# Performance work log

Measured on AMD Instinct MI355X. Metric: run time of the kernel, lower is better.

The kernel has to match this reference:

```python
import jax, jax.numpy as jnp
import numpy as np

IOU_THRESHOLD = 0.7
TOP_K = 100
TAKE_N = 10
EPS = 1e-8


def _iou(proposals, gts):
    # proposals: [B,H,W,A,4] (x1,y1,x2,y2); gts: [G,4] -> iou [B,H,W,G,A]
    p = proposals[:, :, :, None, :, :]          # [B,H,W,1,A,4]
    g = gts[:, None, :]                          # [G,1,4]
    ix1 = jnp.maximum(p[..., 0], g[..., 0])      # [B,H,W,G,A]
    iy1 = jnp.maximum(p[..., 1], g[..., 1])
    ix2 = jnp.minimum(p[..., 2], g[..., 2])
    iy2 = jnp.minimum(p[..., 3], g[..., 3])
    inter = jnp.clip(ix2 - ix1, 0.0) * jnp.clip(iy2 - iy1, 0.0)
    area_p = (p[..., 2] - p[..., 0]) * (p[..., 3] - p[..., 1])
    area_g = (g[..., 2] - g[..., 0]) * (g[..., 3] - g[..., 1])
    return inter / (area_p + area_g - inter + EPS)


def _sample_masked(key, mask, n):
    # uniformly pick n True positions (static shape; pads arbitrarily if < n True)
    score = jnp.where(mask, jax.random.uniform(key, mask.shape), -1.0)
    _, sel = jax.lax.top_k(score, n)
    return sel


def setup_inputs() -> dict:
    key = jax.random.key(0)
    k1, k2, k3, k5 = jax.random.split(key, 4)
    B, H, W, A, G, K = 8, 100, 100, 9, 50, 18
    raw = jax.random.uniform(k1, (B, H, W, A, 4), dtype=jnp.float32)
    xy = raw[..., :2]
    proposals = jnp.concatenate([xy, xy + raw[..., 2:] * 0.2 + 0.01], axis=-1)
    cls_prob = jax.random.uniform(k2, (B, H, W, K), dtype=jnp.float32)
    anchor_prob = jax.random.uniform(k3, (B, H, W, K), dtype=jnp.float32)
    # gt boxes copied from proposals (guarantees some IoU > threshold matches)
    flat = proposals.reshape(-1, 4)
    stride = flat.shape[0] // G
    gt_proposals = flat[::stride][:G]
    gt_cls = jax.random.randint(k5, (G,), 0, 21, dtype=jnp.int32)
    return {"proposals": proposals, "cls_prob": cls_prob, "anchor_prob": anchor_prob,
            "gt_proposals": gt_proposals, "gt_cls": gt_cls}


def reference(proposals, cls_prob, anchor_prob, gt_proposals, gt_cls):
    kp, kn = jax.random.split(jax.random.key(42))
    iou = _iou(proposals, gt_proposals)               # [B,H,W,G,A]
    B, H, W, G, A = iou.shape
    flat_iou = iou.reshape(-1)
    vals, idxs = jax.lax.top_k(flat_iou, TOP_K)
    pos_mask = vals > IOU_THRESHOLD
    sel = _sample_masked(kp, pos_mask, TAKE_N)
    flat_sel = idxs[sel]
    b, h, w, g, a = jnp.unravel_index(flat_sel, iou.shape)
    proposals_index = jnp.stack([b, h, w, g, a], axis=-1)       # [N,5]
    positive_proposals = proposals[b, h, w, a]                  # [N,4]
    positive_cls_prob = cls_prob[b, h, w]                       # [N,K]
    positive_gt_proposals = gt_proposals[g]                     # [N,4]
    positive_gt_cls = gt_cls[g]                                 # [N]
    positive_anchor = a                                         # [N]
    positive_anchor_cls = anchor_prob[b, h, w]                  # [N,K]
    iou_per_position = iou.max(axis=(3, 4))                     # [B,H,W]
    neg_mask = (iou_per_position < IOU_THRESHOLD).reshape(-1)
    nsel = _sample_masked(kn, neg_mask, TAKE_N)
    nb, nh, nw = jnp.unravel_index(nsel, (B, H, W))
    negative_index = jnp.stack([nb, nh, nw], axis=-1)           # [N,3]
    negative_cls_prob = cls_prob[nb, nh, nw]                    # [N,K]
    return (proposals_index, positive_proposals, positive_cls_prob,
            positive_gt_proposals, positive_gt_cls, positive_anchor,
            positive_anchor_cls, negative_index, negative_cls_prob)
```

## Files before the change

kernel.cpp:

```cpp
#include <hip/hip_runtime.h>

constexpr int B = 8, H = 100, W = 100, A = 9, G = 50, K = 18;
constexpr int NPROP = B * H * W * A;
constexpr int NPOS  = B * H * W;
constexpr int CAND_CAP = 65536;
constexpr float THR = 0.7f;

#define JAX_PARTITIONABLE 1

#define TPB 576
#define NB_P 625
#define TPC 512
#define BLK_CAND 1024
#define REFINE_THR 384

__device__ int g_candCount;
__device__ unsigned int g_hist[4096];
__device__ unsigned long long g_cand[CAND_CAP];
__device__ unsigned long long g_negtop[NB_P * 10];

__device__ __forceinline__ unsigned int rotl32(unsigned int x, int r) {
    return (x << r) | (x >> (32 - r));
}
__device__ __forceinline__ void tfr(unsigned int& x0, unsigned int& x1, int r) {
    x0 += x1; x1 = rotl32(x1, r); x1 ^= x0;
}
__device__ void threefry2x32(unsigned int k0, unsigned int k1,
                             unsigned int c0, unsigned int c1,
                             unsigned int& o0, unsigned int& o1) {
    unsigned int ks2 = k0 ^ k1 ^ 0x1BD11BDAu;
    unsigned int x0 = c0 + k0, x1 = c1 + k1;
    tfr(x0,x1,13); tfr(x0,x1,15); tfr(x0,x1,26); tfr(x0,x1, 6);
    x0 += k1;  x1 += ks2 + 1u;
    tfr(x0,x1,17); tfr(x0,x1,29); tfr(x0,x1,16); tfr(x0,x1,24);
    x0 += ks2; x1 += k0 + 2u;
    tfr(x0,x1,13); tfr(x0,x1,15); tfr(x0,x1,26); tfr(x0,x1, 6);
    x0 += k0;  x1 += k1 + 3u;
    tfr(x0,x1,17); tfr(x0,x1,29); tfr(x0,x1,16); tfr(x0,x1,24);
    x0 += k1;  x1 += ks2 + 4u;
    tfr(x0,x1,13); tfr(x0,x1,15); tfr(x0,x1,26); tfr(x0,x1, 6);
    x0 += ks2; x1 += k0 + 5u;
    o0 = x0; o1 = x1;
}

__device__ void derive_keys(unsigned int& kp0, unsigned int& kp1,
                            unsigned int& kn0, unsigned int& kn1) {
#if JAX_PARTITIONABLE
    threefry2x32(0u, 42u, 0u, 0u, kp0, kp1);
    threefry2x32(0u, 42u, 0u, 1u, kn0, kn1);
#else
    unsigned int a0, b0, a1, b1;
    threefry2x32(0u, 42u, 0u, 2u, a0, b0);
    threefry2x32(0u, 42u, 1u, 3u, a1, b1);
    kp0 = a0; kp1 = a1; kn0 = b0; kn1 = b1;
#endif
}

__device__ float jax_uniform(unsigned int k0, unsigned int k1, unsigned int i, unsigned int n) {
    unsigned int bits;
#if JAX_PARTITIONABLE
    unsigned int o0, o1;
    threefry2x32(k0, k1, 0u, i, o0, o1);
    bits = o0 ^ o1;
#else
    unsigned int half = n >> 1;
    unsigned int o0, o1;
    if (i < half) { threefry2x32(k0, k1, i, i + half, o0, o1); bits = o0; }
    else          { threefry2x32(k0, k1, i - half, i, o0, o1); bits = o1; }
#endif
    unsigned int fb = (bits >> 9) | 0x3F800000u;
    return __uint_as_float(fb) - 1.0f;
}

__global__ __launch_bounds__(TPB) void prod_kernel(
        const float* __restrict__ proposals, const float* __restrict__ gtp) {
    __shared__ float  s41[G];
    __shared__ unsigned int sflag[128];
    __shared__ unsigned long long scand[BLK_CAND];
    __shared__ unsigned long long snk[128];
    __shared__ unsigned long long wk[10];
    __shared__ int sh_cnt, sh_base;

    const int t = threadIdx.x;
    const int bid = blockIdx.x;
    const float4* gtp4 = reinterpret_cast<const float4*>(gtp);

    if (t < G) {
        float4 gb = gtp4[t];
        s41[t] = __fmul_rn(0.41f, __fmul_rn(__fsub_rn(gb.z, gb.x), __fsub_rn(gb.w, gb.y)));
    }
    if (t < 128) sflag[t] = 0u;
    if (t == 0) sh_cnt = 0;
    __syncthreads();

    int p0 = bid * 1152 + t;
    float4 x0 = reinterpret_cast<const float4*>(proposals)[p0];
    float4 x1 = reinterpret_cast<const float4*>(proposals)[p0 + 576];
    float ap0 = __fmul_rn(__fsub_rn(x0.z, x0.x), __fsub_rn(x0.w, x0.y));
    float ap1 = __fmul_rn(__fsub_rn(x1.z, x1.x), __fsub_rn(x1.w, x1.y));
    float a41_0 = __fmul_rn(0.41f, ap0);
    float a41_1 = __fmul_rn(0.41f, ap1);
    int li = t / 9, a = t - li * 9;
    int base0 = (bid * 128 + li) * (G * A) + a;
    int base1 = (bid * 128 + 64 + li) * (G * A) + a;
    unsigned f0 = 0u, f1 = 0u;

    for (int g = 0; g < G; ++g) {
        float4 gb = gtp4[g];
        float sg41 = s41[g];
        {
            float dx = __fsub_rn(fminf(x0.z, gb.z), fmaxf(x0.x, gb.x));
            float dy = __fsub_rn(fminf(x0.w, gb.w), fmaxf(x0.y, gb.y));
            float inter = __fmul_rn(fmaxf(dx, 0.0f), fmaxf(dy, 0.0f));
            if (inter > __fadd_rn(a41_0, sg41)) {
                float ag = __fmul_rn(__fsub_rn(gb.z, gb.x), __fsub_rn(gb.w, gb.y));
                float den = __fadd_rn(__fsub_rn(__fadd_rn(ap0, ag), inter), 1e-8f);
                float iou = __fdiv_rn(inter, den);
                if (iou >= THR) f0 = 1u;
                if (iou > THR) {
                    unsigned int delta = __float_as_uint(iou) - 0x3F333334u;
                    unsigned int idx = (unsigned int)(base0 + g * A);
                    unsigned long long key = ((unsigned long long)delta << 32)
                                           | (unsigned long long)(~idx);
                    int s = atomicAdd(&sh_cnt, 1);
                    if (s < BLK_CAND) scand[s] = key;
                    else { int gs = atomicAdd(&g_candCount, 1);
                           if (gs < CAND_CAP) { g_cand[gs] = key;
                               atomicAdd(&g_hist[(unsigned)(key >> 43)], 1u); } }
                }
            }
        }
        {
            float dx = __fsub_rn(fminf(x1.z, gb.z), fmaxf(x1.x, gb.x));
            float dy = __fsub_rn(fminf(x1.w, gb.w), fmaxf(x1.y, gb.y));
            float inter = __fmul_rn(fmaxf(dx, 0.0f), fmaxf(dy, 0.0f));
            if (inter > __fadd_rn(a41_1, sg41)) {
                float ag = __fmul_rn(__fsub_rn(gb.z, gb.x), __fsub_rn(gb.w, gb.y));
                float den = __fadd_rn(__fsub_rn(__fadd_rn(ap1, ag), inter), 1e-8f);
                float iou = __fdiv_rn(inter, den);
                if (iou >= THR) f1 = 1u;
                if (iou > THR) {
                    unsigned int delta = __float_as_uint(iou) - 0x3F333334u;
                    unsigned int idx = (unsigned int)(base1 + g * A);
                    unsigned long long key = ((unsigned long long)delta << 32)
                                           | (unsigned long long)(~idx);
                    int s = atomicAdd(&sh_cnt, 1);
                    if (s < BLK_CAND) scand[s] = key;
                    else { int gs = atomicAdd(&g_candCount, 1);
                           if (gs < CAND_CAP) { g_cand[gs] = key;
                               atomicAdd(&g_hist[(unsigned)(key >> 43)], 1u); } }
                }
            }
        }
    }
    if (f0) atomicOr(&sflag[li], 1u);
    if (f1) atomicOr(&sflag[li + 64], 1u);
    if (t < 10) wk[t] = 0ull;
    __syncthreads();

    int cnt = sh_cnt; if (cnt > BLK_CAND) cnt = BLK_CAND;
    if (t == 0) sh_base = atomicAdd(&g_candCount, cnt);
    if (t < 128) {
        unsigned int kp0, kp1, kn0, kn1;
        derive_keys(kp0, kp1, kn0, kn1);
        unsigned long long key = 0ull;
        if (sflag[t] == 0u) {
            unsigned int pos = (unsigned)(bid * 128 + t);
            float u = jax_uniform(kn0, kn1, pos, (unsigned)NPOS);
            key = ((unsigned long long)__float_as_uint(u) << 32)
                | (unsigned long long)(~pos);
        }
        snk[t] = key;
    }
    __syncthreads();
    int base = sh_base;
    for (int i = t; i < cnt; i += TPB) {
        int gi = base + i;
        if (gi < CAND_CAP) {
            unsigned long long k2 = scand[i];
            g_cand[gi] = k2;
            atomicAdd(&g_hist[(unsigned)(k2 >> 43)], 1u);
        }
    }
    if (t < 128) {
        unsigned long long k2 = snk[t];
        if (k2 != 0ull) {
            int r = 0;
            for (int j = 0; j < 128; ++j) r += (snk[j] > k2) ? 1 : 0;
            if (r < 10) wk[r] = k2;
        }
    }
    __syncthreads();
    if (t < 10) g_negtop[bid * 10 + t] = wk[t];
}

__global__ __launch_bounds__(TPC) void cons_kernel(
        const float* __restrict__ proposals, const float* __restrict__ cls_prob,
        const float* __restrict__ anchor_prob, const float* __restrict__ gtp,
        const int* __restrict__ gtc, float* __restrict__ out) {
    __shared__ unsigned int hist[4096];
    __shared__ int sfx[256];
    __shared__ unsigned long long cbuf[BLK_CAND];
    __shared__ unsigned long long lst[100];
    __shared__ unsigned long long skeys[128];
    __shared__ unsigned long long swin[10];
    __shared__ unsigned long long wred[8];
    __shared__ int selIdx[10];
    __shared__ int s_g[10], s_a[10], s_pos[10], s_bb[10], s_hh[10], s_ww[10], s_npos[10];
    __shared__ int sh_d, sh_before, sh_d2, sh_cnt;

    const int t = threadIdx.x;

    if (blockIdx.x == 0) {
        int C = g_candCount;
        if (C > CAND_CAP) C = CAND_CAP;
        int needTotal = C < 100 ? C : 100;
        int M = 0;

        if (C <= 256) {
            for (int i = t; i < C; i += TPC) cbuf[i] = g_cand[i];
            __syncthreads();
            M = C;
        } else {
            int need = needTotal;
            for (int i = t; i < 4096; i += TPC) hist[i] = g_hist[i];
            __syncthreads();
            if (t < 256) {
                int ps = 0;
                for (int q = 0; q < 16; ++q) ps += (int)hist[t * 16 + q];
                sfx[t] = ps;
            }
            __syncthreads();
            if (t < 64) {
                int lane = t;
                int c0 = sfx[4*lane+0], c1 = sfx[4*lane+1], c2 = sfx[4*lane+2], c3 = sfx[4*lane+3];
                int tot = c0 + c1 + c2 + c3;
                int acc = tot;
                for (int s = 1; s < 64; s <<= 1) {
                    int u = __shfl_down(acc, s);
                    if (lane + s < 64) acc += u;
                }
                int aboveG = acc - tot;
                int CS3 = aboveG;
                int CS2 = CS3 + c3;
                int CS1 = CS2 + c2;
                int CS0 = CS1 + c1;
                int CSv[4] = {CS0, CS1, CS2, CS3};
                int cv[4]  = {c0, c1, c2, c3};
#pragma unroll
                for (int j = 0; j < 4; ++j) {
                    if (CSv[j] < need && CSv[j] + cv[j] >= need) {
                        int cum = CSv[j];
                        for (int b = (4*lane+j)*16 + 15; b >= (4*lane+j)*16; --b) {
                            int h = (int)hist[b];
                            if (cum + h >= need) { sh_d = b; sh_before = cum; break; }
                            cum += h;
                        }
                    }
                }
            }
            __syncthreads();
            int d = sh_d, sb = sh_before;
            int tie = (int)hist[d];
            unsigned long long lo = ((unsigned long long)(unsigned)d) << 43;
            int total = sb + tie;

            if (total > REFINE_THR) {
                __syncthreads();
                for (int i = t; i < 2048; i += TPC) hist[i] = 0u;
                __syncthreads();
                for (int i = t; i < C; i += TPC) {
                    unsigned long long k2 = g_cand[i];
                    if ((unsigned)(k2 >> 43) == (unsigned)d)
                        atomicAdd(&hist[(unsigned)(k2 >> 32) & 0x7FFu], 1u);
                }
                __syncthreads();
                if (t == 0) {
                    int cum = sb;
                    for (int b = 2047; b >= 0; --b) {
                        int h = (int)hist[b];
                        if (cum + h >= need) { sh_d2 = b; break; }
                        cum += h;
                    }
                }
                __syncthreads();
                lo |= ((unsigned long long)(unsigned)sh_d2) << 32;
            }

            if (t == 0) sh_cnt = 0;
            __syncthreads();
            for (int i = t; i < C; i += TPC) {
                unsigned long long k2 = g_cand[i];
                if (k2 >= lo) {
                    int s2 = atomicAdd(&sh_cnt, 1);
                    if (s2 < BLK_CAND) cbuf[s2] = k2;
                }
            }
            __syncthreads();
            M = sh_cnt < BLK_CAND ? sh_cnt : BLK_CAND;
        }

        for (int i = t; i < M; i += TPC) {
            unsigned long long ki = cbuf[i];
            int r = 0;
            for (int j = 0; j < M; ++j) r += (cbuf[j] > ki) ? 1 : 0;
            if (r < needTotal) lst[r] = ki;
        }
        __syncthreads();

        unsigned int kp0, kp1, kn0, kn1;
        derive_keys(kp0, kp1, kn0, kn1);
        if (t < needTotal) {
            float u = jax_uniform(kp0, kp1, (unsigned)t, 100u);
            skeys[t] = ((unsigned long long)__float_as_uint(u) << 32)
                     | (unsigned long long)(~(unsigned)t);
        }
        __syncthreads();
        if (t < needTotal) {
            unsigned long long s = skeys[t];
            int r = 0;
            for (int j = 0; j < needTotal; ++j) r += (skeys[j] > s) ? 1 : 0;
            if (r < 10) selIdx[r] = t;
        }
        __syncthreads();

        if (t < 10) {
            unsigned long long key = lst[selIdx[t]];
            unsigned int fidx = ~(unsigned int)(key & 0xFFFFFFFFull);
            int aa = fidx % A; unsigned int rest = fidx / A;
            int gg = rest % G; rest /= G;
            int ww = rest % W; rest /= W;
            int hh = rest % H; int bb = rest / H;
            s_a[t] = aa; s_g[t] = gg; s_ww[t] = ww; s_hh[t] = hh; s_bb[t] = bb;
            s_pos[t] = (bb * H + hh) * W + ww;
        }
        __syncthreads();

        if (t < 510) {
            int e = t;
            float v;
            if (e < 50)       { int i = e / 5, f = e - 5 * i;
                                v = (float)((f==0)?s_bb[i]:(f==1)?s_hh[i]:(f==2)?s_ww[i]:(f==3)?s_g[i]:s_a[i]); }
            else if (e < 90)  { int u = e - 50, i = u >> 2, q = u & 3;
                                v = proposals[(size_t)(s_pos[i] * A + s_a[i]) * 4 + q]; }
            else if (e < 270) { int u = e - 90, i = u / 18, q = u - 18 * i;
                                v = cls_prob[(size_t)s_pos[i] * K + q]; }
            else if (e < 310) { int u = e - 270, i = u >> 2, q = u & 3;
                                v = gtp[s_g[i] * 4 + q]; }
            else if (e < 320) { v = (float)gtc[s_g[e - 310]]; }
            else if (e < 330) { v = (float)s_a[e - 320]; }
            else              { int u = e - 330, i = u / 18, q = u - 18 * i;
                                v = anchor_prob[(size_t)s_pos[i] * K + q]; }
            out[e] = v;
        }

        __syncthreads();
        for (int i = t; i < 4096; i += TPC) g_hist[i] = 0u;
        if (t == 0) g_candCount = 0;

    } else {
        unsigned long long top[10];
#pragma unroll
        for (int j = 0; j < 10; ++j) top[j] = 0ull;
        for (int i = t; i < NB_P * 10; i += TPC) {
            unsigned long long key = g_negtop[i];
#pragma unroll
            for (int j = 0; j < 10; ++j) {
                if (key > top[j]) { unsigned long long tmp = top[j]; top[j] = key; key = tmp; }
            }
        }
        int lane = t & 63, wid = t >> 6;
        for (int r = 0; r < 10; ++r) {
            unsigned long long w = top[0];
            for (int s = 1; s < 64; s <<= 1) {
                unsigned long long o = __shfl_xor(w, s);
                if (o > w) w = o;
            }
            if (lane == 0) wred[wid] = w;
            __syncthreads();
            unsigned long long m = wred[0];
#pragma unroll
            for (int i = 1; i < 8; ++i) { unsigned long long x = wred[i]; if (x > m) m = x; }
            if (t == 0) swin[r] = m;
            if (top[0] == m) {
#pragma unroll
                for (int j = 0; j < 9; ++j) top[j] = top[j + 1];
                top[9] = 0ull;
            }
            __syncthreads();
        }
        if (t < 10) s_npos[t] = (int)(~(unsigned int)(swin[t] & 0xFFFFFFFFull));
        __syncthreads();

        if (t < 210) {
            int e = 510 + t;
            float v;
            if (e < 540) { int u = e - 510, i = u / 3, f = u - 3 * i; int p = s_npos[i];
                           v = (float)((f==0) ? (p / (H * W)) : (f==1) ? ((p / W) % H) : (p % W)); }
            else         { int u = e - 540, i = u / 18, q = u - 18 * i;
                           v = cls_prob[(size_t)s_npos[i] * K + q]; }
            out[e] = v;
        }
    }
}

extern "C" void kernel_launch(void* const* d_in, const int* in_sizes, int n_in,
                              void* d_out, int out_size, void* d_ws, size_t ws_size,
                              hipStream_t stream) {
    const float* proposals   = (const float*)d_in[0];
    const float* cls_prob    = (const float*)d_in[1];
    const float* anchor_prob = (const float*)d_in[2];
    const float* gtp         = (const float*)d_in[3];
    const int*   gtc         = (const int*)d_in[4];
    float* out = (float*)d_out;

    prod_kernel<<<NB_P, TPB, 0, stream>>>(proposals, gtp);
    cons_kernel<<<2, TPC, 0, stream>>>(proposals, cls_prob, anchor_prob, gtp, gtc, out);
}
```

Before: 44.09 us.

## Fuse producer and consumer into one kernel with binned candidate buckets

Merges the IoU producer kernel and the two-block consumer kernel into a single launch. The extra last block spin-waits on a global completion counter before running the top-k selection. Candidates are now written straight into per-histogram-bin global buckets, replacing the per-block shared staging plus compaction. The consumer therefore scans only the bins at or above the threshold bin instead of the whole candidate list. This removes a kernel launch boundary and the full rescan, at the cost of many global atomics per candidate. It also relies on the waiting block not starving the producers, and the positive and negative selection paths are now serialized in one block.

```diff
diff --git a/kernel.cpp b/kernel.cpp
--- a/kernel.cpp
+++ b/kernel.cpp
@@ -3,20 +3,23 @@
 constexpr int B = 8, H = 100, W = 100, A = 9, G = 50, K = 18;
 constexpr int NPROP = B * H * W * A;
 constexpr int NPOS  = B * H * W;
-constexpr int CAND_CAP = 65536;
 constexpr float THR = 0.7f;
 
 #define JAX_PARTITIONABLE 1
 
 #define TPB 576
 #define NB_P 625
-#define TPC 512
+#define GRID (NB_P + 1)
+#define NBIN 2560
+#define BINCAP 512
+#define SPILL_CAP 16384
 #define BLK_CAND 1024
-#define REFINE_THR 384
-
-__device__ int g_candCount;
-__device__ unsigned int g_hist[4096];
-__device__ unsigned long long g_cand[CAND_CAP];
+
+__device__ unsigned int g_bincnt[NBIN];
+__device__ int g_spillCount;
+__device__ int g_done;
+__device__ unsigned long long g_bins[(size_t)NBIN * BINCAP];
+__device__ unsigned long long g_spill[SPILL_CAP];
 __device__ unsigned long long g_negtop[NB_P * 10];
 
 __device__ __forceinline__ unsigned int rotl32(unsigned int x, int r) {
@@ -72,335 +75,327 @@
     return __uint_as_float(fb) - 1.0f;
 }
 
-__global__ __launch_bounds__(TPB) void prod_kernel(
-        const float* __restrict__ proposals, const float* __restrict__ gtp) {
-    __shared__ float  s41[G];
-    __shared__ unsigned int sflag[128];
-    __shared__ unsigned long long scand[BLK_CAND];
-    __shared__ unsigned long long snk[128];
-    __shared__ unsigned long long wk[10];
-    __shared__ int sh_cnt, sh_base;
-
-    const int t = threadIdx.x;
-    const int bid = blockIdx.x;
-    const float4* gtp4 = reinterpret_cast<const float4*>(gtp);
-
-    if (t < G) {
-        float4 gb = gtp4[t];
-        s41[t] = __fmul_rn(0.41f, __fmul_rn(__fsub_rn(gb.z, gb.x), __fsub_rn(gb.w, gb.y)));
-    }
-    if (t < 128) sflag[t] = 0u;
-    if (t == 0) sh_cnt = 0;
-    __syncthreads();
-
-    int p0 = bid * 1152 + t;
-    float4 x0 = reinterpret_cast<const float4*>(proposals)[p0];
-    float4 x1 = reinterpret_cast<const float4*>(proposals)[p0 + 576];
-    float ap0 = __fmul_rn(__fsub_rn(x0.z, x0.x), __fsub_rn(x0.w, x0.y));
-    float ap1 = __fmul_rn(__fsub_rn(x1.z, x1.x), __fsub_rn(x1.w, x1.y));
-    float a41_0 = __fmul_rn(0.41f, ap0);
-    float a41_1 = __fmul_rn(0.41f, ap1);
-    int li = t / 9, a = t - li * 9;
-    int base0 = (bid * 128 + li) * (G * A) + a;
-    int base1 = (bid * 128 + 64 + li) * (G * A) + a;
-    unsigned f0 = 0u, f1 = 0u;
-
-    for (int g = 0; g < G; ++g) {
-        float4 gb = gtp4[g];
-        float sg41 = s41[g];
-        {
-            float dx = __fsub_rn(fminf(x0.z, gb.z), fmaxf(x0.x, gb.x));
-            float dy = __fsub_rn(fminf(x0.w, gb.w), fmaxf(x0.y, gb.y));
-            float inter = __fmul_rn(fmaxf(dx, 0.0f), fmaxf(dy, 0.0f));
-            if (inter > __fadd_rn(a41_0, sg41)) {
-                float ag = __fmul_rn(__fsub_rn(gb.z, gb.x), __fsub_rn(gb.w, gb.y));
-                float den = __fadd_rn(__fsub_rn(__fadd_rn(ap0, ag), inter), 1e-8f);
-                float iou = __fdiv_rn(inter, den);
-                if (iou >= THR) f0 = 1u;
-                if (iou > THR) {
-                    unsigned int delta = __float_as_uint(iou) - 0x3F333334u;
-                    unsigned int idx = (unsigned int)(base0 + g * A);
-                    unsigned long long key = ((unsigned long long)delta << 32)
-                                           | (unsigned long long)(~idx);
-                    int s = atomicAdd(&sh_cnt, 1);
-                    if (s < BLK_CAND) scand[s] = key;
-                    else { int gs = atomicAdd(&g_candCount, 1);
-                           if (gs < CAND_CAP) { g_cand[gs] = key;
-                               atomicAdd(&g_hist[(unsigned)(key >> 43)], 1u); } }
-                }
-            }
-        }
-        {
-            float dx = __fsub_rn(fminf(x1.z, gb.z), fmaxf(x1.x, gb.x));
-            float dy = __fsub_rn(fminf(x1.w, gb.w), fmaxf(x1.y, gb.y));
-            float inter = __fmul_rn(fmaxf(dx, 0.0f), fmaxf(dy, 0.0f));
-            if (inter > __fadd_rn(a41_1, sg41)) {
-                float ag = __fmul_rn(__fsub_rn(gb.z, gb.x), __fsub_rn(gb.w, gb.y));
-                float den = __fadd_rn(__fsub_rn(__fadd_rn(ap1, ag), inter), 1e-8f);
-                float iou = __fdiv_rn(inter, den);
-                if (iou >= THR) f1 = 1u;
-                if (iou > THR) {
-                    unsigned int delta = __float_as_uint(iou) - 0x3F333334u;
-                    unsigned int idx = (unsigned int)(base1 + g * A);
-                    unsigned long long key = ((unsigned long long)delta << 32)
-                                           | (unsigned long long)(~idx);
-                    int s = atomicAdd(&sh_cnt, 1);
-                    if (s < BLK_CAND) scand[s] = key;
-                    else { int gs = atomicAdd(&g_candCount, 1);
-                           if (gs < CAND_CAP) { g_cand[gs] = key;
-                               atomicAdd(&g_hist[(unsigned)(key >> 43)], 1u); } }
-                }
-            }
-        }
-    }
-    if (f0) atomicOr(&sflag[li], 1u);
-    if (f1) atomicOr(&sflag[li + 64], 1u);
-    if (t < 10) wk[t] = 0ull;
-    __syncthreads();
-
-    int cnt = sh_cnt; if (cnt > BLK_CAND) cnt = BLK_CAND;
-    if (t == 0) sh_base = atomicAdd(&g_candCount, cnt);
-    if (t < 128) {
-        unsigned int kp0, kp1, kn0, kn1;
-        derive_keys(kp0, kp1, kn0, kn1);
-        unsigned long long key = 0ull;
-        if (sflag[t] == 0u) {
-            unsigned int pos = (unsigned)(bid * 128 + t);
-            float u = jax_uniform(kn0, kn1, pos, (unsigned)NPOS);
-            key = ((unsigned long long)__float_as_uint(u) << 32)
-                | (unsigned long long)(~pos);
-        }
-        snk[t] = key;
-    }
-    __syncthreads();
-    int base = sh_base;
-    for (int i = t; i < cnt; i += TPB) {
-        int gi = base + i;
-        if (gi < CAND_CAP) {
-            unsigned long long k2 = scand[i];
-            g_cand[gi] = k2;
-            atomicAdd(&g_hist[(unsigned)(k2 >> 43)], 1u);
-        }
-    }
-    if (t < 128) {
-        unsigned long long k2 = snk[t];
-        if (k2 != 0ull) {
-            int r = 0;
-            for (int j = 0; j < 128; ++j) r += (snk[j] > k2) ? 1 : 0;
-            if (r < 10) wk[r] = k2;
-        }
-    }
-    __syncthreads();
-    if (t < 10) g_negtop[bid * 10 + t] = wk[t];
-}
-
-__global__ __launch_bounds__(TPC) void cons_kernel(
+__device__ __forceinline__ void emit_candidate(float iou, unsigned int idx) {
+    unsigned int delta = __float_as_uint(iou) - 0x3F333334u;
+    unsigned long long key = ((unsigned long long)delta << 32)
+                           | (unsigned long long)(~idx);
+    unsigned int bin = (unsigned int)(key >> 43);
+    unsigned int slot = atomicAdd(&g_bincnt[bin], 1u);
+    if (slot < BINCAP) g_bins[(size_t)bin * BINCAP + slot] = key;
+    else { int gs = atomicAdd(&g_spillCount, 1);
+           if (gs < SPILL_CAP) g_spill[gs] = key; }
+}
+
+__global__ __launch_bounds__(TPB) void fused_kernel(
         const float* __restrict__ proposals, const float* __restrict__ cls_prob,
         const float* __restrict__ anchor_prob, const float* __restrict__ gtp,
         const int* __restrict__ gtc, float* __restrict__ out) {
-    __shared__ unsigned int hist[4096];
+    __shared__ float  s41[G];
+    __shared__ unsigned int sflag[128];
+    __shared__ unsigned long long snk[128];
+    __shared__ unsigned long long wk[10];
+    __shared__ unsigned int hist[NBIN];
     __shared__ int sfx[256];
+    __shared__ unsigned int rhist[2048];
     __shared__ unsigned long long cbuf[BLK_CAND];
     __shared__ unsigned long long lst[100];
     __shared__ unsigned long long skeys[128];
     __shared__ unsigned long long swin[10];
-    __shared__ unsigned long long wred[8];
+    __shared__ unsigned long long wred[9];
     __shared__ int selIdx[10];
     __shared__ int s_g[10], s_a[10], s_pos[10], s_bb[10], s_hh[10], s_ww[10], s_npos[10];
-    __shared__ int sh_d, sh_before, sh_d2, sh_cnt;
+    __shared__ int sh_d, sh_before, sh_C, sh_d2, sh_cnt, sh_ovf;
 
     const int t = threadIdx.x;
-
-    if (blockIdx.x == 0) {
-        int C = g_candCount;
-        if (C > CAND_CAP) C = CAND_CAP;
-        int needTotal = C < 100 ? C : 100;
-        int M = 0;
-
-        if (C <= 256) {
-            for (int i = t; i < C; i += TPC) cbuf[i] = g_cand[i];
-            __syncthreads();
-            M = C;
-        } else {
-            int need = needTotal;
-            for (int i = t; i < 4096; i += TPC) hist[i] = g_hist[i];
-            __syncthreads();
-            if (t < 256) {
-                int ps = 0;
-                for (int q = 0; q < 16; ++q) ps += (int)hist[t * 16 + q];
-                sfx[t] = ps;
-            }
-            __syncthreads();
-            if (t < 64) {
-                int lane = t;
-                int c0 = sfx[4*lane+0], c1 = sfx[4*lane+1], c2 = sfx[4*lane+2], c3 = sfx[4*lane+3];
-                int tot = c0 + c1 + c2 + c3;
-                int acc = tot;
-                for (int s = 1; s < 64; s <<= 1) {
-                    int u = __shfl_down(acc, s);
-                    if (lane + s < 64) acc += u;
+    const int bid = blockIdx.x;
+    const float4* gtp4 = reinterpret_cast<const float4*>(gtp);
+
+    if (bid < NB_P) {
+        if (t < G) {
+            float4 gb = gtp4[t];
+            s41[t] = __fmul_rn(0.41f, __fmul_rn(__fsub_rn(gb.z, gb.x), __fsub_rn(gb.w, gb.y)));
+        }
+        if (t < 128) sflag[t] = 0u;
+        __syncthreads();
+
+        int p0 = bid * 1152 + t;
+        float4 x0 = reinterpret_cast<const float4*>(proposals)[p0];
+        float4 x1 = reinterpret_cast<const float4*>(proposals)[p0 + 576];
+        float ap0 = __fmul_rn(__fsub_rn(x0.z, x0.x), __fsub_rn(x0.w, x0.y));
+        float ap1 = __fmul_rn(__fsub_rn(x1.z, x1.x), __fsub_rn(x1.w, x1.y));
+        float a41_0 = __fmul_rn(0.41f, ap0);
+        float a41_1 = __fmul_rn(0.41f, ap1);
+        int li = t / 9, a = t - li * 9;
+        int base0 = (bid * 128 + li) * (G * A) + a;
+        int base1 = (bid * 128 + 64 + li) * (G * A) + a;
+        unsigned f0 = 0u, f1 = 0u;
+
+        for (int g = 0; g < G; ++g) {
+            float4 gb = gtp4[g];
+            float sg41 = s41[g];
+            {
+                float dx = __fsub_rn(fminf(x0.z, gb.z), fmaxf(x0.x, gb.x));
+                float dy = __fsub_rn(fminf(x0.w, gb.w), fmaxf(x0.y, gb.y));
+                float inter = __fmul_rn(fmaxf(dx, 0.0f), fmaxf(dy, 0.0f));
+                if (inter > __fadd_rn(a41_0, sg41)) {
+                    float ag = __fmul_rn(__fsub_rn(gb.z, gb.x), __fsub_rn(gb.w, gb.y));
+                    float den = __fadd_rn(__fsub_rn(__fadd_rn(ap0, ag), inter), 1e-8f);
+                    float iou = __fdiv_rn(inter, den);
+                    if (iou >= THR) f0 = 1u;
+                    if (iou > THR) emit_candidate(iou, (unsigned int)(base0 + g * A));
                 }
-                int aboveG = acc - tot;
-                int CS3 = aboveG;
-                int CS2 = CS3 + c3;
-                int CS1 = CS2 + c2;
-                int CS0 = CS1 + c1;
-                int CSv[4] = {CS0, CS1, CS2, CS3};
-                int cv[4]  = {c0, c1, c2, c3};
+            }
+            {
+                float dx = __fsub_rn(fminf(x1.z, gb.z), fmaxf(x1.x, gb.x));
+                float dy = __fsub_rn(fminf(x1.w, gb.w), fmaxf(x1.y, gb.y));
+                float inter = __fmul_rn(fmaxf(dx, 0.0f), fmaxf(dy, 0.0f));
+                if (inter > __fadd_rn(a41_1, sg41)) {
+                    float ag = __fmul_rn(__fsub_rn(gb.z, gb.x), __fsub_rn(gb.w, gb.y));
+                    float den = __fadd_rn(__fsub_rn(__fadd_rn(ap1, ag), inter), 1e-8f);
+                    float iou = __fdiv_rn(inter, den);
+                    if (iou >= THR) f1 = 1u;
+                    if (iou > THR) emit_candidate(iou, (unsigned int)(base1 + g * A));
+                }
+            }
+        }
+        if (f0) atomicOr(&sflag[li], 1u);
+        if (f1) atomicOr(&sflag[li + 64], 1u);
+        if (t < 10) wk[t] = 0ull;
+        __syncthreads();
+
+        if (t < 128) {
+            unsigned int kp0, kp1, kn0, kn1;
+            derive_keys(kp0, kp1, kn0, kn1);
+            unsigned long long key = 0ull;
+            if (sflag[t] == 0u) {
+                unsigned int pos = (unsigned)(bid * 128 + t);
+                float u = jax_uniform(kn0, kn1, pos, (unsigned)NPOS);
+                key = ((unsigned long long)__float_as_uint(u) << 32)
+                    | (unsigned long long)(~pos);
+            }
+            snk[t] = key;
+        }
+        __syncthreads();
+        if (t < 128) {
+            unsigned long long k2 = snk[t];
+            if (k2 != 0ull) {
+                int r = 0;
+                for (int j = 0; j < 128; ++j) r += (snk[j] > k2) ? 1 : 0;
+                if (r < 10) wk[r] = k2;
+            }
+        }
+        __syncthreads();
+        if (t < 10) g_negtop[bid * 10 + t] = wk[t];
+        __syncthreads();
+        if (t == 0)
+            __hip_atomic_fetch_add(&g_done, 1, __ATOMIC_RELEASE, __HIP_MEMORY_SCOPE_AGENT);
+        return;
+    }
+
+    if (t == 0) {
+        while (__hip_atomic_load(&g_done, __ATOMIC_ACQUIRE, __HIP_MEMORY_SCOPE_AGENT) < NB_P)
+            __builtin_amdgcn_s_sleep(8);
+    }
+    __syncthreads();
+
+    for (int i = t; i < NBIN; i += TPB) hist[i] = g_bincnt[i];
+    if (t == 0) { sh_d = NBIN - 1; sh_before = 0; sh_ovf = 0; sh_cnt = 0; }
+    __syncthreads();
+    if (t < 256) {
+        int ps = 0;
+        for (int q = 0; q < 10; ++q) ps += (int)hist[t * 10 + q];
+        sfx[t] = ps;
+    }
+    __syncthreads();
+    if (t < 64) {
+        int lane = t;
+        int c0 = sfx[4*lane+0], c1 = sfx[4*lane+1], c2 = sfx[4*lane+2], c3 = sfx[4*lane+3];
+        int tot = c0 + c1 + c2 + c3;
+        int acc = tot;
+        for (int s = 1; s < 64; s <<= 1) {
+            int u = __shfl_down(acc, s);
+            if (lane + s < 64) acc += u;
+        }
+        int C = __shfl(acc, 0);
+        if (lane == 0) sh_C = C;
+        int need = C < 100 ? C : 100;
+        int aboveG = acc - tot;
+        int CS3 = aboveG;
+        int CS2 = CS3 + c3;
+        int CS1 = CS2 + c2;
+        int CS0 = CS1 + c1;
+        int CSv[4] = {CS0, CS1, CS2, CS3};
+        int cv[4]  = {c0, c1, c2, c3};
 #pragma unroll
-                for (int j = 0; j < 4; ++j) {
-                    if (CSv[j] < need && CSv[j] + cv[j] >= need) {
-                        int cum = CSv[j];
-                        for (int b = (4*lane+j)*16 + 15; b >= (4*lane+j)*16; --b) {
-                            int h = (int)hist[b];
-                            if (cum + h >= need) { sh_d = b; sh_before = cum; break; }
-                            cum += h;
-                        }
-                    }
+        for (int j = 0; j < 4; ++j) {
+            if (CSv[j] < need && CSv[j] + cv[j] >= need) {
+                int cum = CSv[j];
+                int cbin = 4*lane + j;
+                for (int b = cbin*10 + 9; b >= cbin*10; --b) {
+                    int h = (int)hist[b];
+                    if (cum + h >= need) { sh_d = b; sh_before = cum; break; }
+                    cum += h;
                 }
             }
-            __syncthreads();
-            int d = sh_d, sb = sh_before;
-            int tie = (int)hist[d];
-            unsigned long long lo = ((unsigned long long)(unsigned)d) << 43;
-            int total = sb + tie;
-
-            if (total > REFINE_THR) {
-                __syncthreads();
-                for (int i = t; i < 2048; i += TPC) hist[i] = 0u;
-                __syncthreads();
-                for (int i = t; i < C; i += TPC) {
-                    unsigned long long k2 = g_cand[i];
-                    if ((unsigned)(k2 >> 43) == (unsigned)d)
-                        atomicAdd(&hist[(unsigned)(k2 >> 32) & 0x7FFu], 1u);
-                }
-                __syncthreads();
-                if (t == 0) {
-                    int cum = sb;
-                    for (int b = 2047; b >= 0; --b) {
-                        int h = (int)hist[b];
-                        if (cum + h >= need) { sh_d2 = b; break; }
-                        cum += h;
-                    }
-                }
-                __syncthreads();
-                lo |= ((unsigned long long)(unsigned)sh_d2) << 32;
-            }
-
-            if (t == 0) sh_cnt = 0;
-            __syncthreads();
-            for (int i = t; i < C; i += TPC) {
-                unsigned long long k2 = g_cand[i];
-                if (k2 >= lo) {
-                    int s2 = atomicAdd(&sh_cnt, 1);
-                    if (s2 < BLK_CAND) cbuf[s2] = k2;
-                }
-            }
-            __syncthreads();
-            M = sh_cnt < BLK_CAND ? sh_cnt : BLK_CAND;
-        }
-
-        for (int i = t; i < M; i += TPC) {
-            unsigned long long ki = cbuf[i];
-            int r = 0;
-            for (int j = 0; j < M; ++j) r += (cbuf[j] > ki) ? 1 : 0;
-            if (r < needTotal) lst[r] = ki;
-        }
-        __syncthreads();
-
-        unsigned int kp0, kp1, kn0, kn1;
-        derive_keys(kp0, kp1, kn0, kn1);
-        if (t < needTotal) {
-            float u = jax_uniform(kp0, kp1, (unsigned)t, 100u);
-            skeys[t] = ((unsigned long long)__float_as_uint(u) << 32)
-                     | (unsigned long long)(~(unsigned)t);
-        }
-        __syncthreads();
-        if (t < needTotal) {
-            unsigned long long s = skeys[t];
-            int r = 0;
-            for (int j = 0; j < needTotal; ++j) r += (skeys[j] > s) ? 1 : 0;
-            if (r < 10) selIdx[r] = t;
-        }
-        __syncthreads();
-
-        if (t < 10) {
-            unsigned long long key = lst[selIdx[t]];
-            unsigned int fidx = ~(unsigned int)(key & 0xFFFFFFFFull);
-            int aa = fidx % A; unsigned int rest = fidx / A;
-            int gg = rest % G; rest /= G;
-            int ww = rest % W; rest /= W;
-            int hh = rest % H; int bb = rest / H;
-            s_a[t] = aa; s_g[t] = gg; s_ww[t] = ww; s_hh[t] = hh; s_bb[t] = bb;
-            s_pos[t] = (bb * H + hh) * W + ww;
-        }
-        __syncthreads();
-
-        if (t < 510) {
-            int e = t;
-            float v;
-            if (e < 50)       { int i = e / 5, f = e - 5 * i;
-                                v = (float)((f==0)?s_bb[i]:(f==1)?s_hh[i]:(f==2)?s_ww[i]:(f==3)?s_g[i]:s_a[i]); }
-            else if (e < 90)  { int u = e - 50, i = u >> 2, q = u & 3;
-                                v = proposals[(size_t)(s_pos[i] * A + s_a[i]) * 4 + q]; }
-            else if (e < 270) { int u = e - 90, i = u / 18, q = u - 18 * i;
-                                v = cls_prob[(size_t)s_pos[i] * K + q]; }
-            else if (e < 310) { int u = e - 270, i = u >> 2, q = u & 3;
-                                v = gtp[s_g[i] * 4 + q]; }
-            else if (e < 320) { v = (float)gtc[s_g[e - 310]]; }
-            else if (e < 330) { v = (float)s_a[e - 320]; }
-            else              { int u = e - 330, i = u / 18, q = u - 18 * i;
-                                v = anchor_prob[(size_t)s_pos[i] * K + q]; }
-            out[e] = v;
-        }
-
-        __syncthreads();
-        for (int i = t; i < 4096; i += TPC) g_hist[i] = 0u;
-        if (t == 0) g_candCount = 0;
-
-    } else {
-        unsigned long long top[10];
+        }
+    }
+    __syncthreads();
+    int C = sh_C;
+    int needTotal = C < 100 ? C : 100;
+    int d = sh_d, sb = sh_before;
+    int tie = (int)hist[d];
+    unsigned long long lo = ((unsigned long long)(unsigned)d) << 43;
+    int spillN = g_spillCount; if (spillN > SPILL_CAP) spillN = SPILL_CAP;
+
+    for (int b = d + t; b < NBIN; b += TPB)
+        if (hist[b] > BINCAP) sh_ovf = 1;
+    __syncthreads();
+
+    if (sb + tie > BLK_CAND) {
+        for (int i = t; i < 2048; i += TPB) rhist[i] = 0u;
+        __syncthreads();
+        int stored_d = tie < BINCAP ? tie : BINCAP;
+        for (int i = t; i < stored_d; i += TPB) {
+            unsigned long long k2 = g_bins[(size_t)d * BINCAP + i];
+            atomicAdd(&rhist[(unsigned)(k2 >> 32) & 0x7FFu], 1u);
+        }
+        if (tie > BINCAP) {
+            for (int i = t; i < spillN; i += TPB) {
+                unsigned long long k2 = g_spill[i];
+                if ((unsigned)(k2 >> 43) == (unsigned)d)
+                    atomicAdd(&rhist[(unsigned)(k2 >> 32) & 0x7FFu], 1u);
+            }
+        }
+        __syncthreads();
+        if (t == 0) {
+            int need = needTotal, cum = sb;
+            sh_d2 = 0;
+            for (int b2 = 2047; b2 >= 0; --b2) {
+                int h2 = (int)rhist[b2];
+                if (cum + h2 >= need) { sh_d2 = b2; break; }
+                cum += h2;
+            }
+        }
+        __syncthreads();
+        lo |= ((unsigned long long)(unsigned)sh_d2) << 32;
+    }
+
+    for (int b = d + t; b < NBIN; b += TPB) {
+        int cnt_b = (int)hist[b]; if (cnt_b > BINCAP) cnt_b = BINCAP;
+        for (int i = 0; i < cnt_b; ++i) {
+            unsigned long long k2 = g_bins[(size_t)b * BINCAP + i];
+            if (k2 >= lo) {
+                int s2 = atomicAdd(&sh_cnt, 1);
+                if (s2 < BLK_CAND) cbuf[s2] = k2;
+            }
+        }
+    }
+    if (sh_ovf) {
+        for (int i = t; i < spillN; i += TPB) {
+            unsigned long long k2 = g_spill[i];
+            if (k2 >= lo) {
+                int s2 = atomicAdd(&sh_cnt, 1);
+                if (s2 < BLK_CAND) cbuf[s2] = k2;
+            }
+        }
+    }
+    __syncthreads();
+    int M = sh_cnt < BLK_CAND ? sh_cnt : BLK_CAND;
+
+    for (int i = t; i < M; i += TPB) {
+        unsigned long long ki = cbuf[i];
+        int r = 0;
+        for (int j = 0; j < M; ++j) r += (cbuf[j] > ki) ? 1 : 0;
+        if (r < needTotal) lst[r] = ki;
+    }
+    __syncthreads();
+
+    unsigned int kp0, kp1, kn0, kn1;
+    derive_keys(kp0, kp1, kn0, kn1);
+    if (t < needTotal) {
+        float u = jax_uniform(kp0, kp1, (unsigned)t, 100u);
+        skeys[t] = ((unsigned long long)__float_as_uint(u) << 32)
+                 | (unsigned long long)(~(unsigned)t);
+    }
+    __syncthreads();
+    if (t < needTotal) {
+        unsigned long long s = skeys[t];
+        int r = 0;
+        for (int j = 0; j < needTotal; ++j) r += (skeys[j] > s) ? 1 : 0;
+        if (r < 10) selIdx[r] = t;
+    }
+    __syncthreads();
+
+    if (t < 10) {
+        unsigned long long key = lst[selIdx[t]];
+        unsigned int fidx = ~(unsigned int)(key & 0xFFFFFFFFull);
+        int aa = fidx % A; unsigned int rest = fidx / A;
+        int gg = rest % G; rest /= G;
+        int ww = rest % W; rest /= W;
+        int hh = rest % H; int bb = rest / H;
+        s_a[t] = aa; s_g[t] = gg; s_ww[t] = ww; s_hh[t] = hh; s_bb[t] = bb;
+        s_pos[t] = (bb * H + hh) * W + ww;
+    }
+
+    unsigned long long top[10];
 #pragma unroll
-        for (int j = 0; j < 10; ++j) top[j] = 0ull;
-        for (int i = t; i < NB_P * 10; i += TPC) {
-            unsigned long long key = g_negtop[i];
+    for (int j = 0; j < 10; ++j) top[j] = 0ull;
+    for (int i = t; i < NB_P * 10; i += TPB) {
+        unsigned long long key = g_negtop[i];
 #pragma unroll
-            for (int j = 0; j < 10; ++j) {
-                if (key > top[j]) { unsigned long long tmp = top[j]; top[j] = key; key = tmp; }
-            }
-        }
-        int lane = t & 63, wid = t >> 6;
-        for (int r = 0; r < 10; ++r) {
-            unsigned long long w = top[0];
-            for (int s = 1; s < 64; s <<= 1) {
-                unsigned long long o = __shfl_xor(w, s);
-                if (o > w) w = o;
-            }
-            if (lane == 0) wred[wid] = w;
-            __syncthreads();
-            unsigned long long m = wred[0];
+        for (int j = 0; j < 10; ++j) {
+            if (key > top[j]) { unsigned long long tmp = top[j]; top[j] = key; key = tmp; }
+        }
+    }
+    int lane = t & 63, wid = t >> 6;
+    for (int r = 0; r < 10; ++r) {
+        unsigned long long w = top[0];
+        for (int s = 1; s < 64; s <<= 1) {
+            unsigned long long o = __shfl_xor(w, s);
+            if (o > w) w = o;
+        }
+        if (lane == 0) wred[wid] = w;
+        __syncthreads();
+        unsigned long long m = wred[0];
 #pragma unroll
-            for (int i = 1; i < 8; ++i) { unsigned long long x = wred[i]; if (x > m) m = x; }
-            if (t == 0) swin[r] = m;
-            if (top[0] == m) {
+        for (int i = 1; i < 9; ++i) { unsigned long long x = wred[i]; if (x > m) m = x; }
+        if (t == 0) swin[r] = m;
+        if (top[0] == m) {
 #pragma unroll
-                for (int j = 0; j < 9; ++j) top[j] = top[j + 1];
-                top[9] = 0ull;
-            }
-            __syncthreads();
-        }
-        if (t < 10) s_npos[t] = (int)(~(unsigned int)(swin[t] & 0xFFFFFFFFull));
-        __syncthreads();
-
-        if (t < 210) {
-            int e = 510 + t;
-            float v;
-            if (e < 540) { int u = e - 510, i = u / 3, f = u - 3 * i; int p = s_npos[i];
-                           v = (float)((f==0) ? (p / (H * W)) : (f==1) ? ((p / W) % H) : (p % W)); }
-            else         { int u = e - 540, i = u / 18, q = u - 18 * i;
-                           v = cls_prob[(size_t)s_npos[i] * K + q]; }
-            out[e] = v;
-        }
+            for (int j = 0; j < 9; ++j) top[j] = top[j + 1];
+            top[9] = 0ull;
+        }
+        __syncthreads();
+    }
+    if (t < 10) s_npos[t] = (int)(~(unsigned int)(swin[t] & 0xFFFFFFFFull));
+    __syncthreads();
+
+    for (int e = t; e < 720; e += TPB) {
+        float v;
+        if (e < 50)       { int i = e / 5, f = e - 5 * i;
+                            v = (float)((f==0)?s_bb[i]:(f==1)?s_hh[i]:(f==2)?s_ww[i]:(f==3)?s_g[i]:s_a[i]); }
+        else if (e < 90)  { int u = e - 50, i = u >> 2, q = u & 3;
+                            v = proposals[(size_t)(s_pos[i] * A + s_a[i]) * 4 + q]; }
+        else if (e < 270) { int u = e - 90, i = u / 18, q = u - 18 * i;
+                            v = cls_prob[(size_t)s_pos[i] * K + q]; }
+        else if (e < 310) { int u = e - 270, i = u >> 2, q = u & 3;
+                            v = gtp[s_g[i] * 4 + q]; }
+        else if (e < 320) { v = (float)gtc[s_g[e - 310]]; }
+        else if (e < 330) { v = (float)s_a[e - 320]; }
+        else if (e < 510) { int u = e - 330, i = u / 18, q = u - 18 * i;
+                            v = anchor_prob[(size_t)s_pos[i] * K + q]; }
+        else if (e < 540) { int u = e - 510, i = u / 3, f = u - 3 * i; int p = s_npos[i];
+                            v = (float)((f==0) ? (p / (H * W)) : (f==1) ? ((p / W) % H) : (p % W)); }
+        else              { int u = e - 540, i = u / 18, q = u - 18 * i;
+                            v = cls_prob[(size_t)s_npos[i] * K + q]; }
+        out[e] = v;
+    }
+
+    __syncthreads();
+    for (int i = t; i < NBIN; i += TPB) g_bincnt[i] = 0u;
+    if (t == 0) {
+        g_spillCount = 0;
+        __hip_atomic_store(&g_done, 0, __ATOMIC_RELEASE, __HIP_MEMORY_SCOPE_AGENT);
     }
 }
 
@@ -414,6 +409,5 @@
     const int*   gtc         = (const int*)d_in[4];
     float* out = (float*)d_out;
 
-    prod_kernel<<<NB_P, TPB, 0, stream>>>(proposals, gtp);
-    cons_kernel<<<2, TPC, 0, stream>>>(proposals, cls_prob, anchor_prob, gtp, gtc, out);
-}
+    fused_kernel<<<GRID, TPB, 0, stream>>>(proposals, cls_prob, anchor_prob, gtp, gtc, out);
+}
```

Result: slower. 65.32 us (+48.2%).
